# Kernel tuning notes

Hardware: AMD Instinct MI355X
Metric: run time of the kernel (lower is better)

## Reference

```python
import jax, jax.numpy as jnp
import numpy as np

N_HEADS, N_LEVELS, N_POINTS = 8, 3, 4


def _bilinear_sample(valf, Hl, Wl, grid):
    """torch.F.grid_sample(mode='bilinear', padding_mode='zeros', align_corners=False).
    valf: [B, nH, hd, Hl*Wl] flattened per-head value map
    grid: [B, Q, nH, P, 2] normalized (x, y) in [-1, 1]
    returns [B, nH, hd, Q, P]
    """
    B, Q, nH, P, _ = grid.shape
    hd = valf.shape[2]
    # unnormalize (align_corners=False)
    ix = ((grid[..., 0] + 1.0) * Wl - 1.0) * 0.5  # [B,Q,nH,P]
    iy = ((grid[..., 1] + 1.0) * Hl - 1.0) * 0.5
    x0 = jnp.floor(ix); y0 = jnp.floor(iy)
    x1 = x0 + 1.0;      y1 = y0 + 1.0
    # corner weights
    w00 = (x1 - ix) * (y1 - iy)
    w01 = (ix - x0) * (y1 - iy)
    w10 = (x1 - ix) * (iy - y0)
    w11 = (ix - x0) * (iy - y0)

    def gather(xi, yi):
        inb = (xi >= 0) & (xi <= Wl - 1) & (yi >= 0) & (yi <= Hl - 1)  # zero padding
        xc = jnp.clip(xi, 0, Wl - 1).astype(jnp.int32)
        yc = jnp.clip(yi, 0, Hl - 1).astype(jnp.int32)
        idx = yc * Wl + xc                              # [B,Q,nH,P]
        idx = idx.transpose(0, 2, 1, 3).reshape(B, nH, 1, Q * P)
        idx = jnp.broadcast_to(idx, (B, nH, hd, Q * P))
        g = jnp.take_along_axis(valf, idx, axis=3)      # [B,nH,hd,Q*P]
        g = g.reshape(B, nH, hd, Q, P)
        mask = inb.transpose(0, 2, 1, 3)[:, :, None, :, :]
        return g * mask

    def w_(w):  # [B,Q,nH,P] -> [B,nH,1,Q,P]
        return w.transpose(0, 2, 1, 3)[:, :, None, :, :]

    return (gather(x0, y0) * w_(w00) + gather(x1, y0) * w_(w01)
            + gather(x0, y1) * w_(w10) + gather(x1, y1) * w_(w11))


def _deform_attn(query, feats, reference_points,
                 W_off, b_off, W_attn, b_attn, W_val, b_val, W_out, b_out):
    B, Q, D = query.shape
    nH, L, P = N_HEADS, N_LEVELS, N_POINTS
    hd = D // nH
    # sampling offsets: tanh * 0.5
    off = jnp.tanh(query @ W_off + b_off).reshape(B, Q, nH, L, P, 2) * 0.5
    # attention weights: softmax over levels*points
    aw = jax.nn.softmax((query @ W_attn + b_attn).reshape(B, Q, nH, L * P), axis=-1)
    aw = aw.reshape(B, Q, nH, L, P)

    out = jnp.zeros((B, Q, nH, hd), dtype=query.dtype)
    for lvl, feat in enumerate(feats):
        Hl, Wl = feat.shape[2], feat.shape[3]
        # value projection on flattened map
        v = feat.reshape(B, D, Hl * Wl).transpose(0, 2, 1) @ W_val + b_val  # [B,S,D]
        valf = v.reshape(B, Hl * Wl, nH, hd).transpose(0, 2, 3, 1)          # [B,nH,hd,S]
        grid = (reference_points[:, :, None, None, :] + off[:, :, :, lvl]) * 2.0 - 1.0  # [B,Q,nH,P,2]
        sampled = _bilinear_sample(valf, Hl, Wl, grid)                      # [B,nH,hd,Q,P]
        w = aw[:, :, :, lvl].transpose(0, 2, 1, 3)[:, :, None, :, :]        # [B,nH,1,Q,P]
        out = out + (sampled * w).sum(-1).transpose(0, 3, 1, 2)             # [B,Q,nH,hd]
    return out.reshape(B, Q, D) @ W_out + b_out


def setup_inputs() -> dict:
    key = jax.random.key(0)
    ks = jax.random.split(key, 13)
    B, Q, D = 4, 8400, 256
    return {
        "query": jax.random.normal(ks[0], (B, Q, D), jnp.float32),
        "feat0": jax.random.normal(ks[1], (B, D, 80, 80), jnp.float32),
        "feat1": jax.random.normal(ks[2], (B, D, 40, 40), jnp.float32),
        "feat2": jax.random.normal(ks[3], (B, D, 20, 20), jnp.float32),
        "reference_points": jax.random.uniform(ks[4], (B, Q, 2), jnp.float32),
        "W_off": jax.random.normal(ks[5], (D, N_HEADS * N_LEVELS * N_POINTS * 2), jnp.float32) * 0.02,
        "b_off": jax.random.normal(ks[6], (N_HEADS * N_LEVELS * N_POINTS * 2,), jnp.float32) * 0.02,
        "W_attn": jax.random.normal(ks[7], (D, N_HEADS * N_LEVELS * N_POINTS), jnp.float32) * 0.02,
        "b_attn": jax.random.normal(ks[8], (N_HEADS * N_LEVELS * N_POINTS,), jnp.float32) * 0.02,
        "W_val": jax.random.normal(ks[9], (D, D), jnp.float32) * (1.0 / np.sqrt(D)),
        "b_val": jnp.zeros((D,), jnp.float32),
        "W_out": jax.random.normal(ks[10], (D, D), jnp.float32) * (1.0 / np.sqrt(D)),
        "b_out": jnp.zeros((D,), jnp.float32),
    }


def reference(query, feat0, feat1, feat2, reference_points,
              W_off, b_off, W_attn, b_attn, W_val, b_val, W_out, b_out):
    return _deform_attn(query, [feat0, feat1, feat2], reference_points,
                        W_off, b_off, W_attn, b_attn, W_val, b_val, W_out, b_out)
```

## Files before the change

kernel.cpp:

```cpp
#include <hip/hip_runtime.h>
#include <math.h>

#define NH    8
#define DIM   256
#define NQ    8400
#define BATCH 4
#define STOT  8400
#define MQ    (BATCH * NQ)

typedef _Float16 f16;
typedef __attribute__((ext_vector_type(2))) _Float16 f16x2;
typedef __attribute__((ext_vector_type(8))) _Float16 f16x8;
typedef __attribute__((ext_vector_type(8))) unsigned short u16x8;
typedef __attribute__((ext_vector_type(4))) float  f32x4;

__global__ __launch_bounds__(256) void prep_all(
    const float* __restrict__ feat0, const float* __restrict__ feat1,
    const float* __restrict__ feat2,
    const float* __restrict__ W_val, const float* __restrict__ W_out,
    const float* __restrict__ W_off, const float* __restrict__ W_attn,
    const float* __restrict__ b_off, const float* __restrict__ b_attn,
    f16* __restrict__ Af, f16* __restrict__ Wvt, f16* __restrict__ Wot,
    f16* __restrict__ Wch, float* __restrict__ bcat)
{
    const int z = blockIdx.z;
    const int t = threadIdx.x;
    __shared__ float tile[32][33];
    const int c = t & 31, r = t >> 5;

    if (z == 4) {
        const int xb = blockIdx.x;
        if (xb > 25) return;
        if (xb == 25) {
            if (blockIdx.y == 0)
                for (int i = t; i < 288; i += 256)
                    bcat[i] = (i < 192) ? b_off[i] : b_attn[i - 192];
            return;
        }
        const float* W; f16* oH; int Nw, n0, nb;
        if (xb < 8)       { W = W_val;  oH = Wvt; Nw = 256; n0 = 0;   nb = xb * 32; }
        else if (xb < 16) { W = W_out;  oH = Wot; Nw = 256; n0 = 0;   nb = (xb - 8) * 32; }
        else if (xb < 22) { W = W_off;  oH = Wch; Nw = 192; n0 = 0;   nb = (xb - 16) * 32; }
        else              { W = W_attn; oH = Wch; Nw = 96;  n0 = 192; nb = (xb - 22) * 32; }
        const int k0 = blockIdx.y * 32;
        #pragma unroll
        for (int i = 0; i < 4; ++i) {
            int k = k0 + r + i * 8, n = nb + c;
            tile[r + i * 8][c] = (n < Nw) ? W[(size_t)k * Nw + n] : 0.f;
        }
        __syncthreads();
        #pragma unroll
        for (int i = 0; i < 4; ++i) {
            int n = nb + r + i * 8, k = k0 + c;
            if (n < Nw)
                oH[(size_t)(n0 + n) * 256 + k] = (f16)tile[c][r + i * 8];
        }
        return;
    }

    const int b = z;
    const int s0 = blockIdx.x * 32, k0 = blockIdx.y * 32;
    if (s0 >= 8400) return;
    const float* f0b = feat0 + (size_t)b * 256 * 6400;
    const float* f1b = feat1 + (size_t)b * 256 * 1600;
    const float* f2b = feat2 + (size_t)b * 256 * 400;
    #pragma unroll
    for (int i = 0; i < 4; ++i) {
        int rr = r + i * 8;
        int s = s0 + c;
        float v = 0.f;
        if (s < 8400) {
            const float* fp; int S, sl;
            if (s < 6400)      { fp = f0b; S = 6400; sl = s; }
            else if (s < 8000) { fp = f1b; S = 1600; sl = s - 6400; }
            else               { fp = f2b; S = 400;  sl = s - 8000; }
            v = fp[(size_t)(k0 + rr) * S + sl];
        }
        tile[rr][c] = v;
    }
    __syncthreads();
    #pragma unroll
    for (int i = 0; i < 4; ++i) {
        int s = s0 + r + i * 8, k = k0 + c;
        if (s < 8400)
            Af[((size_t)b * 8400 + s) * 256 + k] = (f16)tile[c][r + i * 8];
    }
}

__global__ __launch_bounds__(256) void gemm_vr(
    const f16* __restrict__ Af, const float* __restrict__ query,
    const f16* __restrict__ Wvt, const f16* __restrict__ Wch,
    const float* __restrict__ b_val, const float* __restrict__ bcat,
    f16* __restrict__ valh, float* __restrict__ rawo, f16* __restrict__ attnh)
{
    __shared__ unsigned short Ah[128 * 40];
    __shared__ unsigned short Bs[128 * 40];

    const bool split = blockIdx.x >= 2;
    const int bn = split ? (blockIdx.x - 2) * 128 : blockIdx.x * 128;
    const int bm = blockIdx.y * 128;
    const int N = split ? 288 : 256;
    const unsigned short* Bg = (const unsigned short*)(split ? Wch : Wvt);

    const int t = threadIdx.x;
    const int lane = t & 63, w = t >> 6;
    const int wm = (w & 1) * 64, wn = (w >> 1) * 64;
    const int l15 = lane & 15, quad = lane >> 4;

    f32x4 acc[4][4];
    #pragma unroll
    for (int i = 0; i < 4; ++i)
        #pragma unroll
        for (int j = 0; j < 4; ++j)
            acc[i][j] = (f32x4){0.f, 0.f, 0.f, 0.f};

    for (int k0 = 0; k0 < 256; k0 += 32) {
        #pragma unroll
        for (int cc = 0; cc < 2; ++cc) {
            int cid = t + cc * 256;
            int r = cid >> 2, s = cid & 3;
            int gr = bm + r; if (gr > MQ - 1) gr = MQ - 1;
            if (split) {
                const float* ap = query + (size_t)gr * 256 + k0 + s * 8;
                float4 q0 = *(const float4*)ap;
                float4 q1 = *(const float4*)(ap + 4);
                f16x8 hv;
                hv[0] = (f16)q0.x; hv[1] = (f16)q0.y; hv[2] = (f16)q0.z; hv[3] = (f16)q0.w;
                hv[4] = (f16)q1.x; hv[5] = (f16)q1.y; hv[6] = (f16)q1.z; hv[7] = (f16)q1.w;
                *(f16x8*)&Ah[r * 40 + s * 8] = hv;
            } else {
                *(u16x8*)&Ah[r * 40 + s * 8] =
                    *(const u16x8*)((const unsigned short*)Af + (size_t)gr * 256 + k0 + s * 8);
            }
            int gn = bn + r; if (gn > N - 1) gn = N - 1;
            *(u16x8*)&Bs[r * 40 + s * 8] = *(const u16x8*)(Bg + (size_t)gn * 256 + k0 + s * 8);
        }
        __syncthreads();

        f16x8 af[4], bfv[4];
        #pragma unroll
        for (int mt = 0; mt < 4; ++mt)
            af[mt] = *(const f16x8*)&Ah[(wm + mt * 16 + l15) * 40 + quad * 8];
        #pragma unroll
        for (int nt = 0; nt < 4; ++nt)
            bfv[nt] = *(const f16x8*)&Bs[(wn + nt * 16 + l15) * 40 + quad * 8];
        #pragma unroll
        for (int mt = 0; mt < 4; ++mt)
            #pragma unroll
            for (int nt = 0; nt < 4; ++nt)
                acc[mt][nt] = __builtin_amdgcn_mfma_f32_16x16x32_f16(af[mt], bfv[nt], acc[mt][nt], 0, 0, 0);
        __syncthreads();
    }

    #pragma unroll
    for (int nt = 0; nt < 4; ++nt) {
        int col = bn + wn + nt * 16 + l15;
        float bv = (col < N) ? (split ? bcat[col] : b_val[col]) : 0.f;
        #pragma unroll
        for (int mt = 0; mt < 4; ++mt) {
            int row0 = bm + wm + mt * 16 + quad * 4;
            #pragma unroll
            for (int r = 0; r < 4; ++r) {
                int row = row0 + r;
                if (row < MQ && col < N) {
                    float v = acc[mt][nt][r] + bv;
                    if (!split) {
                        int bb = row / STOT, s = row - bb * STOT;
                        int h = col >> 5, c = col & 31;
                        valh[(((size_t)(bb * 8 + h)) * STOT + s) * 32 + c] = (f16)v;
                    } else if (col < 192) {
                        rawo[(size_t)row * 192 + col] = v;
                    } else {
                        attnh[(size_t)row * 96 + (col - 192)] = (f16)v;
                    }
                }
            }
        }
    }
}

__global__ __launch_bounds__(256) void gemm_o(
    const f16* __restrict__ A, const f16* __restrict__ Bt,
    const float* __restrict__ bias, float* __restrict__ C)
{
    __shared__ unsigned short Ah[128 * 40];
    __shared__ unsigned short Bs[128 * 40];
    const int t = threadIdx.x;
    const int bn = blockIdx.x * 128, bm = blockIdx.y * 128;
    const int lane = t & 63, w = t >> 6;
    const int wm = (w & 1) * 64, wn = (w >> 1) * 64;
    const int l15 = lane & 15, quad = lane >> 4;

    f32x4 acc[4][4];
    #pragma unroll
    for (int i = 0; i < 4; ++i)
        #pragma unroll
        for (int j = 0; j < 4; ++j)
            acc[i][j] = (f32x4){0.f, 0.f, 0.f, 0.f};

    for (int k0 = 0; k0 < 256; k0 += 32) {
        #pragma unroll
        for (int cc = 0; cc < 2; ++cc) {
            int cid = t + cc * 256;
            int r = cid >> 2, s = cid & 3;
            int gr = bm + r; if (gr > MQ - 1) gr = MQ - 1;
            *(u16x8*)&Ah[r * 40 + s * 8] = *(const u16x8*)((const unsigned short*)A + (size_t)gr * 256 + k0 + s * 8);
            *(u16x8*)&Bs[r * 40 + s * 8] = *(const u16x8*)((const unsigned short*)Bt + (size_t)(bn + r) * 256 + k0 + s * 8);
        }
        __syncthreads();
        f16x8 af[4], bfv[4];
        #pragma unroll
        for (int mt = 0; mt < 4; ++mt)
            af[mt] = *(const f16x8*)&Ah[(wm + mt * 16 + l15) * 40 + quad * 8];
        #pragma unroll
        for (int nt = 0; nt < 4; ++nt)
            bfv[nt] = *(const f16x8*)&Bs[(wn + nt * 16 + l15) * 40 + quad * 8];
        #pragma unroll
        for (int mt = 0; mt < 4; ++mt)
            #pragma unroll
            for (int nt = 0; nt < 4; ++nt)
                acc[mt][nt] = __builtin_amdgcn_mfma_f32_16x16x32_f16(af[mt], bfv[nt], acc[mt][nt], 0, 0, 0);
        __syncthreads();
    }
    #pragma unroll
    for (int nt = 0; nt < 4; ++nt) {
        int col = bn + wn + nt * 16 + l15;
        float bv = bias[col];
        #pragma unroll
        for (int mt = 0; mt < 4; ++mt) {
            int row0 = bm + wm + mt * 16 + quad * 4;
            #pragma unroll
            for (int r = 0; r < 4; ++r) {
                int row = row0 + r;
                if (row < MQ)
                    C[(size_t)row * 256 + col] = acc[mt][nt][r] + bv;
            }
        }
    }
}

__global__ __launch_bounds__(256) void sample_v6(
    const f16* __restrict__ valh,
    const float* __restrict__ raw_off,
    const f16* __restrict__ attnh,
    const float* __restrict__ refp,
    f16* __restrict__ out_h)
{
    const int bx = blockIdx.x;
    const int xcd = bx & 7;
    const int b = xcd >> 1;
    const int qi = (bx >> 3) * 2 + (xcd & 1);
    const int bq0 = b * NQ + qi * 8;
    const int t = threadIdx.x;

    __shared__ int      s_idx[8][96][4];
    __shared__ unsigned s_wp[8][96][4];
    __shared__ float    s_m[8][8];
    __shared__ float    s_inv[8][8];

    if (t < 64) {
        int q = t >> 3, h = t & 7;
        const f16* a = attnh + (size_t)(bq0 + q) * 96 + h * 12;
        float m = (float)a[0];
        #pragma unroll
        for (int j = 1; j < 12; ++j) m = fmaxf(m, (float)a[j]);
        float s = 0.f;
        #pragma unroll
        for (int j = 0; j < 12; ++j) s += expf((float)a[j] - m);
        s_m[q][h] = m;
        s_inv[q][h] = 1.f / s;
    }
    __syncthreads();

    for (int i = t; i < 768; i += 256) {
        int q = i / 96, p = i - q * 96;
        int h = p / 12, lp = p - h * 12, l = lp >> 2;
        const int dims[3]   = {80, 40, 20};
        const int bases_[3] = {0, 6400, 8000};
        int Wl = dims[l], base = bases_[l];
        float logit = (float)attnh[(size_t)(bq0 + q) * 96 + p];
        float aw = expf(logit - s_m[q][h]) * s_inv[q][h];
        size_t ro = (size_t)(bq0 + q) * 192 + h * 24 + lp * 2;
        float rawx = raw_off[ro], rawy = raw_off[ro + 1];
        float rx = refp[(size_t)(bq0 + q) * 2];
        float ry = refp[(size_t)(bq0 + q) * 2 + 1];
        float ix = (rx + tanhf(rawx) * 0.5f) * Wl - 0.5f;
        float iy = (ry + tanhf(rawy) * 0.5f) * Wl - 0.5f;
        float x0f = floorf(ix), y0f = floorf(iy);
        float fx = ix - x0f, fy = iy - y0f;
        int x0 = (int)x0f, y0 = (int)y0f;
        float w00 = (1.f - fx) * (1.f - fy) * aw;
        float w01 = fx * (1.f - fy) * aw;
        float w10 = (1.f - fx) * fy * aw;
        float w11 = fx * fy * aw;
        bool vx0 = (unsigned)x0 < (unsigned)Wl;
        bool vx1 = (unsigned)(x0 + 1) < (unsigned)Wl;
        bool vy0 = (unsigned)y0 < (unsigned)Wl;
        bool vy1 = (unsigned)(y0 + 1) < (unsigned)Wl;
        int row0 = base + y0 * Wl, row1 = row0 + Wl;
        float ws[4] = { vx0 && vy0 ? w00 : 0.f, vx1 && vy0 ? w01 : 0.f,
                        vx0 && vy1 ? w10 : 0.f, vx1 && vy1 ? w11 : 0.f };
        int   is[4] = { vx0 && vy0 ? row0 + x0 : 0, vx1 && vy0 ? row0 + x0 + 1 : 0,
                        vx0 && vy1 ? row1 + x0 : 0, vx1 && vy1 ? row1 + x0 + 1 : 0 };
        #pragma unroll
        for (int k = 0; k < 4; ++k) {
            unsigned short us = __builtin_bit_cast(unsigned short, (f16)ws[k]);
            s_wp[q][p][k] = ((unsigned)us << 16) | us;
            s_idx[q][p][k] = is[k];
        }
    }
    __syncthreads();

    const int q = t >> 5;
    const int h = (t >> 2) & 7;
    const int l4 = t & 3;
    const uint4* vb4 = (const uint4*)(valh + (size_t)(b * 8 + h) * STOT * 32);
    const int*      ip = &s_idx[q][h * 12][0];
    const unsigned* wp = &s_wp[q][h * 12][0];
    float accf[8] = {};
    #pragma unroll
    for (int pp = 0; pp < 4; ++pp) {
        int ix[12]; unsigned ww[12]; uint4 v[12];
        #pragma unroll
        for (int k = 0; k < 12; ++k) { ix[k] = ip[pp * 12 + k]; ww[k] = wp[pp * 12 + k]; }
        #pragma unroll
        for (int k = 0; k < 12; ++k) v[k] = vb4[(size_t)ix[k] * 4 + l4];
        f16x2 a0 = (f16x2)(f16)0, a1 = a0, a2 = a0, a3 = a0;
        #pragma unroll
        for (int k = 0; k < 12; ++k) {
            f16x2 wv = __builtin_bit_cast(f16x2, ww[k]);
            a0 += wv * __builtin_bit_cast(f16x2, v[k].x);
            a1 += wv * __builtin_bit_cast(f16x2, v[k].y);
            a2 += wv * __builtin_bit_cast(f16x2, v[k].z);
            a3 += wv * __builtin_bit_cast(f16x2, v[k].w);
        }
        accf[0] += (float)a0[0]; accf[1] += (float)a0[1];
        accf[2] += (float)a1[0]; accf[3] += (float)a1[1];
        accf[4] += (float)a2[0]; accf[5] += (float)a2[1];
        accf[6] += (float)a3[0]; accf[7] += (float)a3[1];
    }
    f16x8 ob;
    #pragma unroll
    for (int c = 0; c < 8; ++c) ob[c] = (f16)accf[c];
    *(f16x8*)(out_h + (size_t)(bq0 + q) * 256 + h * 32 + l4 * 8) = ob;
}

extern "C" void kernel_launch(void* const* d_in, const int* in_sizes, int n_in,
                              void* d_out, int out_size, void* d_ws, size_t ws_size,
                              hipStream_t stream)
{
    const float* query  = (const float*)d_in[0];
    const float* feat0  = (const float*)d_in[1];
    const float* feat1  = (const float*)d_in[2];
    const float* feat2  = (const float*)d_in[3];
    const float* refp   = (const float*)d_in[4];
    const float* W_off  = (const float*)d_in[5];
    const float* b_off  = (const float*)d_in[6];
    const float* W_attn = (const float*)d_in[7];
    const float* b_attn = (const float*)d_in[8];
    const float* W_val  = (const float*)d_in[9];
    const float* b_val  = (const float*)d_in[10];
    const float* W_out  = (const float*)d_in[11];
    const float* b_out  = (const float*)d_in[12];
    float* out = (float*)d_out;

    f16*   valh  = (f16*)d_ws;
    float* rawo  = (float*)(valh + (size_t)MQ * 256);
    f16*   attnh = (f16*)(rawo + (size_t)MQ * 192);
    f16*   Af    = attnh + (size_t)MQ * 96;
    f16*   outh  = Af;
    f16*   Wvt   = Af + (size_t)MQ * 256;
    f16*   Wot   = Wvt + 65536;
    f16*   Wch   = Wot + 65536;
    float* bcat  = (float*)(Wch + 73728);

    dim3 blk(256);

    prep_all<<<dim3(263, 8, 5), blk, 0, stream>>>(feat0, feat1, feat2,
                                                  W_val, W_out, W_off, W_attn,
                                                  b_off, b_attn,
                                                  Af, Wvt, Wot, Wch, bcat);
    gemm_vr<<<dim3(5, 263), blk, 0, stream>>>(Af, query, Wvt, Wch, b_val, bcat,
                                              valh, rawo, attnh);
    sample_v6<<<dim3(MQ / 8), blk, 0, stream>>>(valh, rawo, attnh, refp, outh);
    gemm_o<<<dim3(2, 263), blk, 0, stream>>>(outh, Wot, b_out, out);
}
```

Before: 251.3 us.

## Load GEMM tiles directly into LDS with XOR swizzle and prequantize query

Both GEMMs now stage their A and B tiles with global_load_lds (direct global-to-LDS copies) instead of loading through registers. The padded LDS layout is replaced by an XOR-swizzled 32-wide layout to avoid bank conflicts. Because a direct copy cannot convert types, the fp32 query is converted to fp16 in a new prep_all slice and written to an extra workspace buffer. This adds an extra read and write pass over the query in exchange for cheaper, conversion-free tile staging in the GEMMs.

```diff
diff --git a/kernel.cpp b/kernel.cpp
--- a/kernel.cpp
+++ b/kernel.cpp
@@ -14,19 +14,43 @@
 typedef __attribute__((ext_vector_type(8))) unsigned short u16x8;
 typedef __attribute__((ext_vector_type(4))) float  f32x4;
 
+static __device__ __forceinline__ void gl_lds16(const void* g, void* l) {
+    __builtin_amdgcn_global_load_lds(
+        (const __attribute__((address_space(1))) unsigned int*)g,
+        (__attribute__((address_space(3))) unsigned int*)(unsigned int)(unsigned long long)l,
+        16, 0, 0);
+}
+
 __global__ __launch_bounds__(256) void prep_all(
     const float* __restrict__ feat0, const float* __restrict__ feat1,
-    const float* __restrict__ feat2,
+    const float* __restrict__ feat2, const float* __restrict__ query,
     const float* __restrict__ W_val, const float* __restrict__ W_out,
     const float* __restrict__ W_off, const float* __restrict__ W_attn,
     const float* __restrict__ b_off, const float* __restrict__ b_attn,
-    f16* __restrict__ Af, f16* __restrict__ Wvt, f16* __restrict__ Wot,
+    f16* __restrict__ Af, f16* __restrict__ Qh,
+    f16* __restrict__ Wvt, f16* __restrict__ Wot,
     f16* __restrict__ Wch, float* __restrict__ bcat)
 {
     const int z = blockIdx.z;
     const int t = threadIdx.x;
     __shared__ float tile[32][33];
     const int c = t & 31, r = t >> 5;
+
+    if (z == 5) {
+        size_t base = ((size_t)(blockIdx.x * 8 + blockIdx.y) * 256 + t) * 16;
+        if (base < (size_t)MQ * 256) {
+            #pragma unroll
+            for (int i = 0; i < 2; ++i) {
+                float4 q0 = *(const float4*)(query + base + i * 8);
+                float4 q1 = *(const float4*)(query + base + i * 8 + 4);
+                f16x8 hv;
+                hv[0] = (f16)q0.x; hv[1] = (f16)q0.y; hv[2] = (f16)q0.z; hv[3] = (f16)q0.w;
+                hv[4] = (f16)q1.x; hv[5] = (f16)q1.y; hv[6] = (f16)q1.z; hv[7] = (f16)q1.w;
+                *(f16x8*)(Qh + base + i * 8) = hv;
+            }
+        }
+        return;
+    }
 
     if (z == 4) {
         const int xb = blockIdx.x;
@@ -87,26 +111,35 @@
     }
 }
 
-__global__ __launch_bounds__(256) void gemm_vr(
-    const f16* __restrict__ Af, const float* __restrict__ query,
-    const f16* __restrict__ Wvt, const f16* __restrict__ Wch,
-    const float* __restrict__ b_val, const float* __restrict__ bcat,
-    f16* __restrict__ valh, float* __restrict__ rawo, f16* __restrict__ attnh)
+template<int KIND>
+__global__ __launch_bounds__(256) void gemm_glds(
+    const f16* __restrict__ A0, const f16* __restrict__ A1,
+    const f16* __restrict__ B0, const f16* __restrict__ B1,
+    const float* __restrict__ bias0, const float* __restrict__ bias1,
+    f16* __restrict__ valh, float* __restrict__ rawo, f16* __restrict__ attnh,
+    float* __restrict__ Cf)
 {
-    __shared__ unsigned short Ah[128 * 40];
-    __shared__ unsigned short Bs[128 * 40];
-
-    const bool split = blockIdx.x >= 2;
+    __shared__ f16 Ah[128 * 32];
+    __shared__ f16 Bs[128 * 32];
+
+    const bool split = (KIND == 0) && (blockIdx.x >= 2);
     const int bn = split ? (blockIdx.x - 2) * 128 : blockIdx.x * 128;
     const int bm = blockIdx.y * 128;
     const int N = split ? 288 : 256;
-    const unsigned short* Bg = (const unsigned short*)(split ? Wch : Wvt);
+    const f16* Ag = split ? A1 : A0;
+    const f16* Bg = split ? B1 : B0;
+    const float* bias = split ? bias1 : bias0;
 
     const int t = threadIdx.x;
     const int lane = t & 63, w = t >> 6;
     const int wm = (w & 1) * 64, wn = (w >> 1) * 64;
     const int l15 = lane & 15, quad = lane >> 4;
 
+    const int fstage = ((t >> 2) & 3) ^ ((t >> 4) & 3);
+    const int qs = (t & 3) ^ fstage;
+    const int ffrag = (l15 & 3) ^ ((l15 >> 2) & 3);
+    const int qf = quad ^ ffrag;
+
     f32x4 acc[4][4];
     #pragma unroll
     for (int i = 0; i < 4; ++i)
@@ -116,34 +149,23 @@
 
     for (int k0 = 0; k0 < 256; k0 += 32) {
         #pragma unroll
-        for (int cc = 0; cc < 2; ++cc) {
-            int cid = t + cc * 256;
-            int r = cid >> 2, s = cid & 3;
-            int gr = bm + r; if (gr > MQ - 1) gr = MQ - 1;
-            if (split) {
-                const float* ap = query + (size_t)gr * 256 + k0 + s * 8;
-                float4 q0 = *(const float4*)ap;
-                float4 q1 = *(const float4*)(ap + 4);
-                f16x8 hv;
-                hv[0] = (f16)q0.x; hv[1] = (f16)q0.y; hv[2] = (f16)q0.z; hv[3] = (f16)q0.w;
-                hv[4] = (f16)q1.x; hv[5] = (f16)q1.y; hv[6] = (f16)q1.z; hv[7] = (f16)q1.w;
-                *(f16x8*)&Ah[r * 40 + s * 8] = hv;
-            } else {
-                *(u16x8*)&Ah[r * 40 + s * 8] =
-                    *(const u16x8*)((const unsigned short*)Af + (size_t)gr * 256 + k0 + s * 8);
-            }
-            int gn = bn + r; if (gn > N - 1) gn = N - 1;
-            *(u16x8*)&Bs[r * 40 + s * 8] = *(const u16x8*)(Bg + (size_t)gn * 256 + k0 + s * 8);
+        for (int i = 0; i < 2; ++i) {
+            int row = i * 64 + (t >> 2);
+            int slot = i * 256 + t;
+            int gr = bm + row; if (gr > MQ - 1) gr = MQ - 1;
+            gl_lds16(Ag + (size_t)gr * 256 + k0 + qs * 8, &Ah[slot * 8]);
+            int gn = bn + row; if (gn > N - 1) gn = N - 1;
+            gl_lds16(Bg + (size_t)gn * 256 + k0 + qs * 8, &Bs[slot * 8]);
         }
         __syncthreads();
 
         f16x8 af[4], bfv[4];
         #pragma unroll
         for (int mt = 0; mt < 4; ++mt)
-            af[mt] = *(const f16x8*)&Ah[(wm + mt * 16 + l15) * 40 + quad * 8];
+            af[mt] = *(const f16x8*)&Ah[((wm + mt * 16 + l15) * 4 + qf) * 8];
         #pragma unroll
         for (int nt = 0; nt < 4; ++nt)
-            bfv[nt] = *(const f16x8*)&Bs[(wn + nt * 16 + l15) * 40 + quad * 8];
+            bfv[nt] = *(const f16x8*)&Bs[((wn + nt * 16 + l15) * 4 + qf) * 8];
         #pragma unroll
         for (int mt = 0; mt < 4; ++mt)
             #pragma unroll
@@ -155,85 +177,26 @@
     #pragma unroll
     for (int nt = 0; nt < 4; ++nt) {
         int col = bn + wn + nt * 16 + l15;
-        float bv = (col < N) ? (split ? bcat[col] : b_val[col]) : 0.f;
+        float bv = (col < N) ? bias[col] : 0.f;
         #pragma unroll
         for (int mt = 0; mt < 4; ++mt) {
             int row0 = bm + wm + mt * 16 + quad * 4;
             #pragma unroll
             for (int r = 0; r < 4; ++r) {
                 int row = row0 + r;
-                if (row < MQ && col < N) {
-                    float v = acc[mt][nt][r] + bv;
-                    if (!split) {
-                        int bb = row / STOT, s = row - bb * STOT;
-                        int h = col >> 5, c = col & 31;
-                        valh[(((size_t)(bb * 8 + h)) * STOT + s) * 32 + c] = (f16)v;
-                    } else if (col < 192) {
-                        rawo[(size_t)row * 192 + col] = v;
-                    } else {
-                        attnh[(size_t)row * 96 + (col - 192)] = (f16)v;
-                    }
+                if (row >= MQ || col >= N) continue;
+                float v = acc[mt][nt][r] + bv;
+                if (KIND == 1) {
+                    Cf[(size_t)row * 256 + col] = v;
+                } else if (!split) {
+                    int bb = row / STOT, s = row - bb * STOT;
+                    int h = col >> 5, c = col & 31;
+                    valh[(((size_t)(bb * 8 + h)) * STOT + s) * 32 + c] = (f16)v;
+                } else if (col < 192) {
+                    rawo[(size_t)row * 192 + col] = v;
+                } else {
+                    attnh[(size_t)row * 96 + (col - 192)] = (f16)v;
                 }
-            }
-        }
-    }
-}
-
-__global__ __launch_bounds__(256) void gemm_o(
-    const f16* __restrict__ A, const f16* __restrict__ Bt,
-    const float* __restrict__ bias, float* __restrict__ C)
-{
-    __shared__ unsigned short Ah[128 * 40];
-    __shared__ unsigned short Bs[128 * 40];
-    const int t = threadIdx.x;
-    const int bn = blockIdx.x * 128, bm = blockIdx.y * 128;
-    const int lane = t & 63, w = t >> 6;
-    const int wm = (w & 1) * 64, wn = (w >> 1) * 64;
-    const int l15 = lane & 15, quad = lane >> 4;
-
-    f32x4 acc[4][4];
-    #pragma unroll
-    for (int i = 0; i < 4; ++i)
-        #pragma unroll
-        for (int j = 0; j < 4; ++j)
-            acc[i][j] = (f32x4){0.f, 0.f, 0.f, 0.f};
-
-    for (int k0 = 0; k0 < 256; k0 += 32) {
-        #pragma unroll
-        for (int cc = 0; cc < 2; ++cc) {
-            int cid = t + cc * 256;
-            int r = cid >> 2, s = cid & 3;
-            int gr = bm + r; if (gr > MQ - 1) gr = MQ - 1;
-            *(u16x8*)&Ah[r * 40 + s * 8] = *(const u16x8*)((const unsigned short*)A + (size_t)gr * 256 + k0 + s * 8);
-            *(u16x8*)&Bs[r * 40 + s * 8] = *(const u16x8*)((const unsigned short*)Bt + (size_t)(bn + r) * 256 + k0 + s * 8);
-        }
-        __syncthreads();
-        f16x8 af[4], bfv[4];
-        #pragma unroll
-        for (int mt = 0; mt < 4; ++mt)
-            af[mt] = *(const f16x8*)&Ah[(wm + mt * 16 + l15) * 40 + quad * 8];
-        #pragma unroll
-        for (int nt = 0; nt < 4; ++nt)
-            bfv[nt] = *(const f16x8*)&Bs[(wn + nt * 16 + l15) * 40 + quad * 8];
-        #pragma unroll
-        for (int mt = 0; mt < 4; ++mt)
-            #pragma unroll
-            for (int nt = 0; nt < 4; ++nt)
-                acc[mt][nt] = __builtin_amdgcn_mfma_f32_16x16x32_f16(af[mt], bfv[nt], acc[mt][nt], 0, 0, 0);
-        __syncthreads();
-    }
-    #pragma unroll
-    for (int nt = 0; nt < 4; ++nt) {
-        int col = bn + wn + nt * 16 + l15;
-        float bv = bias[col];
-        #pragma unroll
-        for (int mt = 0; mt < 4; ++mt) {
-            int row0 = bm + wm + mt * 16 + quad * 4;
-            #pragma unroll
-            for (int r = 0; r < 4; ++r) {
-                int row = row0 + r;
-                if (row < MQ)
-                    C[(size_t)row * 256 + col] = acc[mt][nt][r] + bv;
             }
         }
     }
@@ -369,19 +332,22 @@
     f16*   attnh = (f16*)(rawo + (size_t)MQ * 192);
     f16*   Af    = attnh + (size_t)MQ * 96;
     f16*   outh  = Af;
-    f16*   Wvt   = Af + (size_t)MQ * 256;
+    f16*   Qh    = Af + (size_t)MQ * 256;
+    f16*   Wvt   = Qh + (size_t)MQ * 256;
     f16*   Wot   = Wvt + 65536;
     f16*   Wch   = Wot + 65536;
     float* bcat  = (float*)(Wch + 73728);
 
     dim3 blk(256);
 
-    prep_all<<<dim3(263, 8, 5), blk, 0, stream>>>(feat0, feat1, feat2,
+    prep_all<<<dim3(263, 8, 6), blk, 0, stream>>>(feat0, feat1, feat2, query,
                                                   W_val, W_out, W_off, W_attn,
                                                   b_off, b_attn,
-                                                  Af, Wvt, Wot, Wch, bcat);
-    gemm_vr<<<dim3(5, 263), blk, 0, stream>>>(Af, query, Wvt, Wch, b_val, bcat,
-                                              valh, rawo, attnh);
+                                                  Af, Qh, Wvt, Wot, Wch, bcat);
+    gemm_glds<0><<<dim3(5, 263), blk, 0, stream>>>(Af, Qh, Wvt, Wch, b_val, bcat,
+                                                   valh, rawo, attnh, nullptr);
     sample_v6<<<dim3(MQ / 8), blk, 0, stream>>>(valh, rawo, attnh, refp, outh);
-    gemm_o<<<dim3(2, 263), blk, 0, stream>>>(outh, Wot, b_out, out);
-}
+    gemm_glds<1><<<dim3(2, 263), blk, 0, stream>>>(outh, nullptr, Wot, nullptr,
+                                                   b_out, nullptr,
+                                                   nullptr, nullptr, nullptr, out);
+}
```

Measured after the change: 239.2 us. 4.8% less time.
